# Kernel optimization log

Hardware: AMD Instinct MI355X
Metric: run time of the kernel (lower is better)

Reference implementation:

```python
import jax, jax.numpy as jnp
import numpy as np


def setup_inputs() -> dict:
    key = jax.random.key(0)
    k1, k2 = jax.random.split(key)
    B, N, X, Y, Z = 1, 96, 128, 128, 64
    embedding = jax.random.normal(k1, (B, 3, X, Y, Z), dtype=jnp.float32)
    centroids = jax.random.uniform(k2, (B, N, 3), dtype=jnp.float32)  # max <= 1 -> no /scale
    sigma = jnp.ones((3,), dtype=jnp.float32)
    scale = jnp.full((3,), 25.0, dtype=jnp.float32)  # self.scale from __init__ default 25
    return {"embedding": embedding, "centroids": centroids, "sigma": sigma, "scale": scale}


def reference(embedding, centroids, sigma, scale):
    # embedding: [B,3,X,Y,Z], centroids: [B,N,3], sigma: [3], scale: [3]
    sigma = sigma + 1e-10
    # centroids = centroids / scale if centroids.max() > 5 (pixel coords -> normalized)
    centroids = jnp.where(jnp.max(centroids) > 5.0, centroids / scale, centroids)
    denom = 2.0 * sigma * sigma  # [3], = sigma.pow(2).mul(2)
    # Fused across all N centroids (original loops over n):
    # diff2: [B,N,3,X,Y,Z]
    diff2 = (embedding[:, None, :, :, :, :] - centroids[:, :, :, None, None, None]) ** 2
    logp = -(diff2 / denom[None, None, :, None, None, None]).sum(axis=2)  # [B,N,X,Y,Z]
    return jnp.exp(logp)
```

## Files before the change

### kernel.cpp

```cpp
#include <hip/hip_runtime.h>


typedef float f32x4 __attribute__((ext_vector_type(4)));

#define LOG2E 1.4426950408889634f

constexpr int  N_CENT  = 96;
constexpr long V_TOT   = 128L * 128 * 64;
constexpr int  NCHUNK  = 8;
constexpr long V_CHUNK = V_TOT / NCHUNK;
constexpr int  BLK     = 256;
constexpr int  VPT     = 4;
constexpr int  ITERS   = (int)(V_CHUNK / (BLK * VPT));

__global__ __launch_bounds__(BLK)
void e2p_kernel(const float* __restrict__ emb,
                const float* __restrict__ cent,
                const float* __restrict__ sigma,
                float* __restrict__ out)
{
    const int n     = blockIdx.x >> 3;
    const int chunk = blockIdx.x & 7;

    const float s0 = sigma[0] + 1e-10f;
    const float s1 = sigma[1] + 1e-10f;
    const float s2 = sigma[2] + 1e-10f;
    const float g0 = LOG2E / (2.0f * s0 * s0);
    const float g1 = LOG2E / (2.0f * s1 * s1);
    const float g2 = LOG2E / (2.0f * s2 * s2);

    const float c0 = cent[n * 3 + 0];
    const float c1 = cent[n * 3 + 1];
    const float c2 = cent[n * 3 + 2];
    const float A0 = 2.0f * c0 * g0;
    const float A1 = 2.0f * c1 * g1;
    const float A2 = 2.0f * c2 * g2;
    const float Bc = -(c0 * c0 * g0 + c1 * c1 * g1 + c2 * c2 * g2);

    const long vbase = chunk * V_CHUNK + (long)threadIdx.x * VPT;

    const float* p0 = emb + vbase;
    const float* p1 = emb + V_TOT + vbase;
    const float* p2 = emb + 2 * V_TOT + vbase;
    float*       o  = out + (long)n * V_TOT + vbase;

    constexpr long STEP = (long)BLK * VPT;

    for (int i = 0; i < ITERS; ++i) {
        const f32x4 e0 = *(const f32x4*)p0;
        const f32x4 e1 = *(const f32x4*)p1;
        const f32x4 e2 = *(const f32x4*)p2;

        f32x4 r;
        #pragma unroll
        for (int j = 0; j < 4; ++j) {
            float acc = fmaf(fmaf(-g0, e0[j], A0), e0[j], Bc);
            acc       = fmaf(fmaf(-g1, e1[j], A1), e1[j], acc);
            acc       = fmaf(fmaf(-g2, e2[j], A2), e2[j], acc);
            r[j] = __builtin_amdgcn_exp2f(acc);
        }
        __builtin_nontemporal_store(r, (f32x4*)o);

        p0 += STEP; p1 += STEP; p2 += STEP; o += STEP;
    }
}

extern "C" void kernel_launch(void* const* d_in, const int* in_sizes, int n_in,
                              void* d_out, int out_size, void* d_ws, size_t ws_size,
                              hipStream_t stream)
{
    const float* emb   = (const float*)d_in[0];
    const float* cent  = (const float*)d_in[1];
    const float* sigma = (const float*)d_in[2];
    float* out = (float*)d_out;

    const int blocks = N_CENT * NCHUNK;
    e2p_kernel<<<blocks, BLK, 0, stream>>>(emb, cent, sigma, out);
}
```

Before: 84.46 us.

## Batch four vec4 loads per thread, enlarge blocks, use regular stores

```diff
diff --git a/kernel.cpp b/kernel.cpp
--- a/kernel.cpp
+++ b/kernel.cpp
@@ -9,9 +9,10 @@
 constexpr long V_TOT   = 128L * 128 * 64;
 constexpr int  NCHUNK  = 8;
 constexpr long V_CHUNK = V_TOT / NCHUNK;
-constexpr int  BLK     = 256;
-constexpr int  VPT     = 4;
-constexpr int  ITERS   = (int)(V_CHUNK / (BLK * VPT));
+constexpr int  BLK     = 512;
+constexpr int  NV4     = 4;
+constexpr long STEP    = (long)BLK * 4 * NV4;
+constexpr int  ITERS   = (int)(V_CHUNK / STEP);
 
 __global__ __launch_bounds__(BLK)
 void e2p_kernel(const float* __restrict__ emb,
@@ -37,29 +38,37 @@
     const float A2 = 2.0f * c2 * g2;
     const float Bc = -(c0 * c0 * g0 + c1 * c1 * g1 + c2 * c2 * g2);
 
-    const long vbase = chunk * V_CHUNK + (long)threadIdx.x * VPT;
+    const long vbase = chunk * V_CHUNK + (long)threadIdx.x * 4;
 
     const float* p0 = emb + vbase;
     const float* p1 = emb + V_TOT + vbase;
     const float* p2 = emb + 2 * V_TOT + vbase;
     float*       o  = out + (long)n * V_TOT + vbase;
 
-    constexpr long STEP = (long)BLK * VPT;
+    for (int i = 0; i < ITERS; ++i) {
+        f32x4 e0[NV4], e1[NV4], e2[NV4];
+        #pragma unroll
+        for (int k = 0; k < NV4; ++k) {
+            e0[k] = *(const f32x4*)(p0 + (long)k * BLK * 4);
+            e1[k] = *(const f32x4*)(p1 + (long)k * BLK * 4);
+            e2[k] = *(const f32x4*)(p2 + (long)k * BLK * 4);
+        }
 
-    for (int i = 0; i < ITERS; ++i) {
-        const f32x4 e0 = *(const f32x4*)p0;
-        const f32x4 e1 = *(const f32x4*)p1;
-        const f32x4 e2 = *(const f32x4*)p2;
+        f32x4 r[NV4];
+        #pragma unroll
+        for (int k = 0; k < NV4; ++k) {
+            #pragma unroll
+            for (int j = 0; j < 4; ++j) {
+                float acc = fmaf(fmaf(-g0, e0[k][j], A0), e0[k][j], Bc);
+                acc       = fmaf(fmaf(-g1, e1[k][j], A1), e1[k][j], acc);
+                acc       = fmaf(fmaf(-g2, e2[k][j], A2), e2[k][j], acc);
+                r[k][j] = __builtin_amdgcn_exp2f(acc);
+            }
+        }
 
-        f32x4 r;
         #pragma unroll
-        for (int j = 0; j < 4; ++j) {
-            float acc = fmaf(fmaf(-g0, e0[j], A0), e0[j], Bc);
-            acc       = fmaf(fmaf(-g1, e1[j], A1), e1[j], acc);
-            acc       = fmaf(fmaf(-g2, e2[j], A2), e2[j], acc);
-            r[j] = __builtin_amdgcn_exp2f(acc);
-        }
-        __builtin_nontemporal_store(r, (f32x4*)o);
+        for (int k = 0; k < NV4; ++k)
+            *(f32x4*)(o + (long)k * BLK * 4) = r[k];
 
         p0 += STEP; p1 += STEP; p2 += STEP; o += STEP;
     }
```

After: 126.9 us. 1.5x slower.
